# Performance work log

Hardware: AMD Instinct MI355X
Metric: run time of the kernel (lower is better)

Reference implementation:

```python
import jax, jax.numpy as jnp
import numpy as np


def setup_inputs() -> dict:
    key = jax.random.key(0)
    k1, k2 = jax.random.split(key)
    inputs = jax.random.normal(k1, (32, 4096, 64), dtype=jnp.float32)
    embed = jax.random.normal(k2, (64, 1024), dtype=jnp.float32)  # [embed_dim, n_embed]
    return {"inputs": inputs, "embed": embed}


def reference(inputs, embed):
    # Eval-mode forward of VectorQuantizer (self.training == False, no EMA update).
    embed_dim, n_embed = embed.shape
    flat = inputs.reshape(-1, embed_dim)  # [N, D]
    # distances[n, k] = ||flat_n||^2 - 2 flat_n . e_k + ||e_k||^2
    distances = (
        jnp.sum(flat * flat, axis=1, keepdims=True)
        - 2.0 * (flat @ embed)
        + jnp.sum(embed * embed, axis=0, keepdims=True)
    )  # [N, n_embed]
    # torch.argmax(-distances, 1) == argmin(distances, 1) (same first-occurrence tie-break)
    encoding_indices = jnp.argmin(distances, axis=1)  # [N] int
    idx = encoding_indices.reshape(inputs.shape[:-1])  # [B, T]
    # quantize: F.embedding(idx, embed.T) -> gather rows of embed.T
    quantized = jnp.take(embed.T, idx, axis=0)  # [B, T, D]
    codes = jnp.concatenate([inputs, quantized], axis=-1)  # [B, T, 2D]
    # straight-through estimator
    quantized_st = inputs + jax.lax.stop_gradient(quantized - inputs)
    return quantized_st, codes, idx
```

## Files before the change

### kernel.cpp

```cpp
#include <hip/hip_runtime.h>

#define D 64
#define KCODES 1024
#define PTS_PER_BLK 256
#define MTILES 16
#define NT 16
#define WL_CAP 8192

typedef short bf16x8 __attribute__((ext_vector_type(8)));
typedef float f32x4 __attribute__((ext_vector_type(4)));

static __device__ __forceinline__ short f2bf(float f) {
  unsigned u = __float_as_uint(f);
  u += 0x7FFF + ((u >> 16) & 1);
  return (short)(u >> 16);
}

static __device__ __forceinline__ void evalExact(const float* __restrict__ inputs,
                                                 const float* __restrict__ embedT,
                                                 const float* __restrict__ en2,
                                                 const float* __restrict__ fn2,
                                                 int p0blk, int pl, int c,
                                                 unsigned long long* s_best) {
  int p = p0blk + pl;
  const float* f = inputs + (size_t)p * D;
  const float* e = embedT + (size_t)c * D;
  float a0 = 0.f, a1 = 0.f, a2 = 0.f, a3 = 0.f;
#pragma unroll
  for (int d = 0; d < D; d += 4) {
    a0 = fmaf(f[d + 0], e[d + 0], a0);
    a1 = fmaf(f[d + 1], e[d + 1], a1);
    a2 = fmaf(f[d + 2], e[d + 2], a2);
    a3 = fmaf(f[d + 3], e[d + 3], a3);
  }
  float dot = (a0 + a1) + (a2 + a3);
  float dist = fmaf(-2.f, dot, fn2[p]) + en2[c];
  unsigned long long key = ((unsigned long long)__float_as_uint(dist) << 32) | (unsigned)c;
  atomicMin(&s_best[pl], key);
}

__global__ void __launch_bounds__(256) vq_prep_codes(const float* __restrict__ embed,
                                                     float* __restrict__ embedT,
                                                     unsigned short* __restrict__ embedTb,
                                                     float* __restrict__ en2,
                                                     int* __restrict__ en2max_bits) {
  int k = blockIdx.x * 256 + threadIdx.x;
  float row[D];
  float s = 0.f;
#pragma unroll
  for (int d = 0; d < D; ++d) {
    float e = embed[d * KCODES + k];
    row[d] = e;
    s = fmaf(e, e, s);
  }
  en2[k] = s;
  float4* o4 = reinterpret_cast<float4*>(embedT + (size_t)k * D);
#pragma unroll
  for (int j = 0; j < 16; ++j)
    o4[j] = make_float4(row[4 * j], row[4 * j + 1], row[4 * j + 2], row[4 * j + 3]);
  unsigned us[32];
#pragma unroll
  for (int j = 0; j < 32; ++j) {
    unsigned lo = (unsigned short)f2bf(row[2 * j]);
    unsigned hi = (unsigned short)f2bf(row[2 * j + 1]);
    us[j] = lo | (hi << 16);
  }
  uint4* ob = reinterpret_cast<uint4*>(embedTb + (size_t)k * D);
#pragma unroll
  for (int j = 0; j < 8; ++j) ob[j] = make_uint4(us[4 * j], us[4 * j + 1], us[4 * j + 2], us[4 * j + 3]);
  float m = s;
#pragma unroll
  for (int off = 32; off; off >>= 1) m = fmaxf(m, __shfl_down(m, off, 64));
  if ((threadIdx.x & 63) == 0) atomicMax(en2max_bits, __float_as_int(m));
}

__global__ void __launch_bounds__(256) vq_prep_fn2(const float* __restrict__ inputs,
                                                   float* __restrict__ fn2) {
  int p = blockIdx.x * 256 + threadIdx.x;
  const float4* i4 = reinterpret_cast<const float4*>(inputs + (size_t)p * D);
  float s = 0.f;
#pragma unroll
  for (int j = 0; j < 16; ++j) {
    float4 v = i4[j];
    s = fmaf(v.x, v.x, s); s = fmaf(v.y, v.y, s);
    s = fmaf(v.z, v.z, s); s = fmaf(v.w, v.w, s);
  }
  fn2[p] = s;
}

__global__ void __launch_bounds__(256, 2) vq_main_kernel(
    const float* __restrict__ inputs, const float* __restrict__ embedT,
    const unsigned short* __restrict__ embedTb, const float* __restrict__ en2,
    const float* __restrict__ fn2, const int* __restrict__ en2max_bits,
    float* __restrict__ out_q, float* __restrict__ out_codes,
    float* __restrict__ out_idx) {
  __shared__ unsigned long long s_best[PTS_PER_BLK];
  __shared__ unsigned s_wl[WL_CAP];
  __shared__ int s_wcount;
  __shared__ float s_wmin[4][16];

  const int tid = threadIdx.x;
  const int w = tid >> 6;
  const int l = tid & 63;
  const int l15 = l & 15;
  const int lg = l >> 4;
  const int p0blk = blockIdx.x * PTS_PER_BLK;
  const int cbase = w * 256;

  s_best[tid] = ~0ull;
  if (tid == 0) s_wcount = 0;

  const float en2max = __int_as_float(*en2max_bits);

  bf16x8 bfr[NT][2];
#pragma unroll
  for (int t = 0; t < NT; ++t) {
    const bf16x8* bp = reinterpret_cast<const bf16x8*>(
        embedTb + (size_t)(cbase + 16 * t + l15) * D + lg * 8);
    bfr[t][0] = bp[0];
    bfr[t][1] = bp[4];
  }
  float en2v[NT];
#pragma unroll
  for (int t = 0; t < NT; ++t) en2v[t] = en2[cbase + 16 * t + l15];

  __syncthreads();

#pragma unroll 1
  for (int mt = 0; mt < MTILES; ++mt) {
    const int p0 = p0blk + mt * 16;
    const float* arow = inputs + (size_t)(p0 + l15) * D + lg * 8;
    f32x4 acc[NT];
#pragma unroll
    for (int t = 0; t < NT; ++t) acc[t] = (f32x4){0.f, 0.f, 0.f, 0.f};
#pragma unroll
    for (int kf = 0; kf < 2; ++kf) {
      float4 a0 = *reinterpret_cast<const float4*>(arow + kf * 32);
      float4 a1 = *reinterpret_cast<const float4*>(arow + kf * 32 + 4);
      bf16x8 af;
      af[0] = f2bf(a0.x); af[1] = f2bf(a0.y); af[2] = f2bf(a0.z); af[3] = f2bf(a0.w);
      af[4] = f2bf(a1.x); af[5] = f2bf(a1.y); af[6] = f2bf(a1.z); af[7] = f2bf(a1.w);
#pragma unroll
      for (int t = 0; t < NT; ++t)
        acc[t] = __builtin_amdgcn_mfma_f32_16x16x32_bf16(af, bfr[t][kf], acc[t], 0, 0, 0);
    }
    float fnv[4];
#pragma unroll
    for (int r = 0; r < 4; ++r) fnv[r] = fn2[p0 + lg * 4 + r];
#pragma unroll
    for (int t = 0; t < NT; ++t)
#pragma unroll
      for (int r = 0; r < 4; ++r)
        acc[t][r] = fmaf(-2.f, acc[t][r], fnv[r]) + en2v[t];

    float m[4];
#pragma unroll
    for (int r = 0; r < 4; ++r) {
      float mm = acc[0][r];
#pragma unroll
      for (int t = 1; t < NT; ++t) mm = fminf(mm, acc[t][r]);
#pragma unroll
      for (int s = 1; s < 16; s <<= 1) mm = fminf(mm, __shfl_xor(mm, s, 16));
      m[r] = mm;
    }
    if (l15 == 0) {
#pragma unroll
      for (int r = 0; r < 4; ++r) s_wmin[w][lg * 4 + r] = m[r];
    }
    __syncthreads();
    float thr[4];
#pragma unroll
    for (int r = 0; r < 4; ++r) {
      int q = lg * 4 + r;
      float fm = fminf(fminf(s_wmin[0][q], s_wmin[1][q]), fminf(s_wmin[2][q], s_wmin[3][q]));
      thr[r] = fm + (0.03125f * sqrtf(fnv[r] * en2max) + 0.01f);
    }
#pragma unroll
    for (int t = 0; t < NT; ++t)
#pragma unroll
      for (int r = 0; r < 4; ++r)
        if (acc[t][r] <= thr[r]) {
          int pl = mt * 16 + lg * 4 + r;
          int c = cbase + 16 * t + l15;
          int pos = atomicAdd(&s_wcount, 1);
          if (pos < WL_CAP) s_wl[pos] = (unsigned)((pl << 10) | c);
          else evalExact(inputs, embedT, en2, fn2, p0blk, pl, c, s_best);
        }
    __syncthreads();
  }

  int wc = s_wcount; if (wc > WL_CAP) wc = WL_CAP;
  for (int i = tid; i < wc; i += 256)
    evalExact(inputs, embedT, en2, fn2, p0blk, (int)(s_wl[i] >> 10), (int)(s_wl[i] & 1023), s_best);
  __syncthreads();

  const int sub = tid & 3;
#pragma unroll 1
  for (int pass = 0; pass < 4; ++pass) {
    int pl = pass * 64 + (tid >> 2);
    unsigned long long key = s_best[pl];
    int c = (int)(unsigned)(key & 0xFFFFFFFFu);
    int p = p0blk + pl;
    const float4* qrow = reinterpret_cast<const float4*>(embedT + (size_t)c * D);
    const float4* frow = reinterpret_cast<const float4*>(inputs + (size_t)p * D);
    float4* oq = reinterpret_cast<float4*>(out_q + (size_t)p * D);
    float4* oc = reinterpret_cast<float4*>(out_codes + (size_t)p * 2 * D);
#pragma unroll
    for (int j = 0; j < 4; ++j) {
      int i4 = j * 4 + sub;
      float4 qv = qrow[i4];
      float4 fv = frow[i4];
      oq[i4] = qv;
      oc[i4] = fv;
      oc[16 + i4] = qv;
    }
    if (sub == 0) out_idx[p] = (float)c;
  }
}

extern "C" void kernel_launch(void* const* d_in, const int* in_sizes, int n_in,
                              void* d_out, int out_size, void* d_ws, size_t ws_size,
                              hipStream_t stream) {
  const float* inputs = (const float*)d_in[0];
  const float* embed  = (const float*)d_in[1];
  int N = in_sizes[0] / D;

  float* embedT          = (float*)d_ws;
  unsigned short* embedTb = (unsigned short*)(embedT + KCODES * D);
  float* en2             = (float*)(embedTb + KCODES * D);
  float* fn2             = en2 + KCODES;
  int* en2max_bits       = (int*)(fn2 + N);

  float* out = (float*)d_out;
  float* out_q     = out;
  float* out_codes = out + (size_t)N * D;
  float* out_idx   = out + (size_t)N * D * 3;

  vq_prep_codes<<<KCODES / 256, 256, 0, stream>>>(embed, embedT, embedTb, en2, en2max_bits);
  vq_prep_fn2<<<N / 256, 256, 0, stream>>>(inputs, fn2);
  vq_main_kernel<<<N / PTS_PER_BLK, 256, 0, stream>>>(inputs, embedT, embedTb, en2, fn2,
                                                      en2max_bits, out_q, out_codes, out_idx);
}
```

Before: 310.5 us.

## Fuse input-norm prep into main kernel, drop per-tile block barriers, prefetch A tiles

Removes the separate input-norm kernel and computes the per-point squared norms into shared memory at the start of the main kernel. It replaces the cross-wave min reduction, which needed two block barriers per M tile, with a per-wave threshold, so each wave filters candidates independently. It also software-prefetches the next tile's input rows into registers and uses nontemporal stores for the outputs. The per-wave threshold is looser, so more candidates may reach the exact-evaluation worklist, and the extra prefetch registers may raise register pressure.

```diff
diff --git a/kernel.cpp b/kernel.cpp
--- a/kernel.cpp
+++ b/kernel.cpp
@@ -19,7 +19,7 @@
 static __device__ __forceinline__ void evalExact(const float* __restrict__ inputs,
                                                  const float* __restrict__ embedT,
                                                  const float* __restrict__ en2,
-                                                 const float* __restrict__ fn2,
+                                                 const float* s_fn2,
                                                  int p0blk, int pl, int c,
                                                  unsigned long long* s_best) {
   int p = p0blk + pl;
@@ -34,7 +34,7 @@
     a3 = fmaf(f[d + 3], e[d + 3], a3);
   }
   float dot = (a0 + a1) + (a2 + a3);
-  float dist = fmaf(-2.f, dot, fn2[p]) + en2[c];
+  float dist = fmaf(-2.f, dot, s_fn2[pl]) + en2[c];
   unsigned long long key = ((unsigned long long)__float_as_uint(dist) << 32) | (unsigned)c;
   atomicMin(&s_best[pl], key);
 }
@@ -74,30 +74,16 @@
   if ((threadIdx.x & 63) == 0) atomicMax(en2max_bits, __float_as_int(m));
 }
 
-__global__ void __launch_bounds__(256) vq_prep_fn2(const float* __restrict__ inputs,
-                                                   float* __restrict__ fn2) {
-  int p = blockIdx.x * 256 + threadIdx.x;
-  const float4* i4 = reinterpret_cast<const float4*>(inputs + (size_t)p * D);
-  float s = 0.f;
-#pragma unroll
-  for (int j = 0; j < 16; ++j) {
-    float4 v = i4[j];
-    s = fmaf(v.x, v.x, s); s = fmaf(v.y, v.y, s);
-    s = fmaf(v.z, v.z, s); s = fmaf(v.w, v.w, s);
-  }
-  fn2[p] = s;
-}
-
 __global__ void __launch_bounds__(256, 2) vq_main_kernel(
     const float* __restrict__ inputs, const float* __restrict__ embedT,
     const unsigned short* __restrict__ embedTb, const float* __restrict__ en2,
-    const float* __restrict__ fn2, const int* __restrict__ en2max_bits,
+    const int* __restrict__ en2max_bits,
     float* __restrict__ out_q, float* __restrict__ out_codes,
     float* __restrict__ out_idx) {
   __shared__ unsigned long long s_best[PTS_PER_BLK];
   __shared__ unsigned s_wl[WL_CAP];
   __shared__ int s_wcount;
-  __shared__ float s_wmin[4][16];
+  __shared__ float s_fn2[PTS_PER_BLK];
 
   const int tid = threadIdx.x;
   const int w = tid >> 6;
@@ -110,6 +96,18 @@
   s_best[tid] = ~0ull;
   if (tid == 0) s_wcount = 0;
 
+  {
+    const float4* i4 = reinterpret_cast<const float4*>(inputs + (size_t)(p0blk + tid) * D);
+    float s = 0.f;
+#pragma unroll
+    for (int j = 0; j < 16; ++j) {
+      float4 v = i4[j];
+      s = fmaf(v.x, v.x, s); s = fmaf(v.y, v.y, s);
+      s = fmaf(v.z, v.z, s); s = fmaf(v.w, v.w, s);
+    }
+    s_fn2[tid] = s;
+  }
+
   const float en2max = __int_as_float(*en2max_bits);
 
   bf16x8 bfr[NT][2];
@@ -126,34 +124,50 @@
 
   __syncthreads();
 
+  float4 A0, A1, A2, A3;
+  {
+    const float* arow = inputs + (size_t)(p0blk + l15) * D + lg * 8;
+    A0 = *reinterpret_cast<const float4*>(arow + 0);
+    A1 = *reinterpret_cast<const float4*>(arow + 4);
+    A2 = *reinterpret_cast<const float4*>(arow + 32);
+    A3 = *reinterpret_cast<const float4*>(arow + 36);
+  }
+
 #pragma unroll 1
   for (int mt = 0; mt < MTILES; ++mt) {
-    const int p0 = p0blk + mt * 16;
-    const float* arow = inputs + (size_t)(p0 + l15) * D + lg * 8;
+    const int mtn = (mt + 1 < MTILES) ? mt + 1 : mt;
+    const float* an = inputs + (size_t)(p0blk + mtn * 16 + l15) * D + lg * 8;
+    float4 N0 = *reinterpret_cast<const float4*>(an + 0);
+    float4 N1 = *reinterpret_cast<const float4*>(an + 4);
+    float4 N2 = *reinterpret_cast<const float4*>(an + 32);
+    float4 N3 = *reinterpret_cast<const float4*>(an + 36);
+
+    bf16x8 af0, af1;
+    af0[0] = f2bf(A0.x); af0[1] = f2bf(A0.y); af0[2] = f2bf(A0.z); af0[3] = f2bf(A0.w);
+    af0[4] = f2bf(A1.x); af0[5] = f2bf(A1.y); af0[6] = f2bf(A1.z); af0[7] = f2bf(A1.w);
+    af1[0] = f2bf(A2.x); af1[1] = f2bf(A2.y); af1[2] = f2bf(A2.z); af1[3] = f2bf(A2.w);
+    af1[4] = f2bf(A3.x); af1[5] = f2bf(A3.y); af1[6] = f2bf(A3.z); af1[7] = f2bf(A3.w);
+
     f32x4 acc[NT];
 #pragma unroll
     for (int t = 0; t < NT; ++t) acc[t] = (f32x4){0.f, 0.f, 0.f, 0.f};
 #pragma unroll
-    for (int kf = 0; kf < 2; ++kf) {
-      float4 a0 = *reinterpret_cast<const float4*>(arow + kf * 32);
-      float4 a1 = *reinterpret_cast<const float4*>(arow + kf * 32 + 4);
-      bf16x8 af;
-      af[0] = f2bf(a0.x); af[1] = f2bf(a0.y); af[2] = f2bf(a0.z); af[3] = f2bf(a0.w);
-      af[4] = f2bf(a1.x); af[5] = f2bf(a1.y); af[6] = f2bf(a1.z); af[7] = f2bf(a1.w);
-#pragma unroll
-      for (int t = 0; t < NT; ++t)
-        acc[t] = __builtin_amdgcn_mfma_f32_16x16x32_bf16(af, bfr[t][kf], acc[t], 0, 0, 0);
-    }
+    for (int t = 0; t < NT; ++t)
+      acc[t] = __builtin_amdgcn_mfma_f32_16x16x32_bf16(af0, bfr[t][0], acc[t], 0, 0, 0);
+#pragma unroll
+    for (int t = 0; t < NT; ++t)
+      acc[t] = __builtin_amdgcn_mfma_f32_16x16x32_bf16(af1, bfr[t][1], acc[t], 0, 0, 0);
+
     float fnv[4];
 #pragma unroll
-    for (int r = 0; r < 4; ++r) fnv[r] = fn2[p0 + lg * 4 + r];
+    for (int r = 0; r < 4; ++r) fnv[r] = s_fn2[mt * 16 + lg * 4 + r];
 #pragma unroll
     for (int t = 0; t < NT; ++t)
 #pragma unroll
       for (int r = 0; r < 4; ++r)
         acc[t][r] = fmaf(-2.f, acc[t][r], fnv[r]) + en2v[t];
 
-    float m[4];
+    float thr[4];
 #pragma unroll
     for (int r = 0; r < 4; ++r) {
       float mm = acc[0][r];
@@ -161,19 +175,7 @@
       for (int t = 1; t < NT; ++t) mm = fminf(mm, acc[t][r]);
 #pragma unroll
       for (int s = 1; s < 16; s <<= 1) mm = fminf(mm, __shfl_xor(mm, s, 16));
-      m[r] = mm;
-    }
-    if (l15 == 0) {
-#pragma unroll
-      for (int r = 0; r < 4; ++r) s_wmin[w][lg * 4 + r] = m[r];
-    }
-    __syncthreads();
-    float thr[4];
-#pragma unroll
-    for (int r = 0; r < 4; ++r) {
-      int q = lg * 4 + r;
-      float fm = fminf(fminf(s_wmin[0][q], s_wmin[1][q]), fminf(s_wmin[2][q], s_wmin[3][q]));
-      thr[r] = fm + (0.03125f * sqrtf(fnv[r] * en2max) + 0.01f);
+      thr[r] = mm + (0.03125f * sqrtf(fnv[r] * en2max) + 0.01f);
     }
 #pragma unroll
     for (int t = 0; t < NT; ++t)
@@ -184,14 +186,17 @@
           int c = cbase + 16 * t + l15;
           int pos = atomicAdd(&s_wcount, 1);
           if (pos < WL_CAP) s_wl[pos] = (unsigned)((pl << 10) | c);
-          else evalExact(inputs, embedT, en2, fn2, p0blk, pl, c, s_best);
+          else evalExact(inputs, embedT, en2, s_fn2, p0blk, pl, c, s_best);
         }
-    __syncthreads();
-  }
+
+    A0 = N0; A1 = N1; A2 = N2; A3 = N3;
+  }
+
+  __syncthreads();
 
   int wc = s_wcount; if (wc > WL_CAP) wc = WL_CAP;
   for (int i = tid; i < wc; i += 256)
-    evalExact(inputs, embedT, en2, fn2, p0blk, (int)(s_wl[i] >> 10), (int)(s_wl[i] & 1023), s_best);
+    evalExact(inputs, embedT, en2, s_fn2, p0blk, (int)(s_wl[i] >> 10), (int)(s_wl[i] & 1023), s_best);
   __syncthreads();
 
   const int sub = tid & 3;
@@ -201,20 +206,20 @@
     unsigned long long key = s_best[pl];
     int c = (int)(unsigned)(key & 0xFFFFFFFFu);
     int p = p0blk + pl;
-    const float4* qrow = reinterpret_cast<const float4*>(embedT + (size_t)c * D);
-    const float4* frow = reinterpret_cast<const float4*>(inputs + (size_t)p * D);
-    float4* oq = reinterpret_cast<float4*>(out_q + (size_t)p * D);
-    float4* oc = reinterpret_cast<float4*>(out_codes + (size_t)p * 2 * D);
+    const f32x4* qrow = reinterpret_cast<const f32x4*>(embedT + (size_t)c * D);
+    const f32x4* frow = reinterpret_cast<const f32x4*>(inputs + (size_t)p * D);
+    f32x4* oq = reinterpret_cast<f32x4*>(out_q + (size_t)p * D);
+    f32x4* oc = reinterpret_cast<f32x4*>(out_codes + (size_t)p * 2 * D);
 #pragma unroll
     for (int j = 0; j < 4; ++j) {
       int i4 = j * 4 + sub;
-      float4 qv = qrow[i4];
-      float4 fv = frow[i4];
-      oq[i4] = qv;
-      oc[i4] = fv;
-      oc[16 + i4] = qv;
+      f32x4 qv = qrow[i4];
+      f32x4 fv = frow[i4];
+      __builtin_nontemporal_store(qv, &oq[i4]);
+      __builtin_nontemporal_store(fv, &oc[i4]);
+      __builtin_nontemporal_store(qv, &oc[16 + i4]);
     }
-    if (sub == 0) out_idx[p] = (float)c;
+    if (sub == 0) __builtin_nontemporal_store((float)c, &out_idx[p]);
   }
 }
 
@@ -228,8 +233,8 @@
   float* embedT          = (float*)d_ws;
   unsigned short* embedTb = (unsigned short*)(embedT + KCODES * D);
   float* en2             = (float*)(embedTb + KCODES * D);
-  float* fn2             = en2 + KCODES;
-  int* en2max_bits       = (int*)(fn2 + N);
+  float* fn2_unused      = en2 + KCODES;
+  int* en2max_bits       = (int*)(fn2_unused + N);
 
   float* out = (float*)d_out;
   float* out_q     = out;
@@ -237,7 +242,6 @@
   float* out_idx   = out + (size_t)N * D * 3;
 
   vq_prep_codes<<<KCODES / 256, 256, 0, stream>>>(embed, embedT, embedTb, en2, en2max_bits);
-  vq_prep_fn2<<<N / 256, 256, 0, stream>>>(inputs, fn2);
-  vq_main_kernel<<<N / PTS_PER_BLK, 256, 0, stream>>>(inputs, embedT, embedTb, en2, fn2,
+  vq_main_kernel<<<N / PTS_PER_BLK, 256, 0, stream>>>(inputs, embedT, embedTb, en2,
                                                       en2max_bits, out_q, out_codes, out_idx);
 }
```

New measurement: 314.2 us. Within noise of the previous version (+1.2%).
